# Kernel optimization log

Hardware: AMD Instinct MI355X
Metric: run time of the kernel (lower is better)

## Reference

```python
import jax, jax.numpy as jnp
import numpy as np
import math

TOPK = 13
ALPHA = 1.0
BETA = 6.0
EPS = 1e-9
NUM_CLASSES = 80
BG = NUM_CLASSES
IMG = 640.0


def _make_centers():
    # YOLO-style anchor-free grid at strides 8/16/32 for a 640x640 image -> L=8400
    pts = []
    for s, g in [(8, 80), (16, 40), (32, 20)]:
        xs = (np.arange(g) + 0.5) * s
        xv, yv = np.meshgrid(xs, xs)
        pts.append(np.stack([xv.ravel(), yv.ravel()], axis=-1))
    return jnp.asarray(np.concatenate(pts, 0), jnp.float32)


def _rand_boxes(kc, kw, shape, wmin, wmax):
    c = jax.random.uniform(kc, shape + (2,), minval=0.0, maxval=IMG)
    wh = jax.random.uniform(kw, shape + (2,), minval=wmin, maxval=wmax)
    return jnp.concatenate([c - wh / 2, c + wh / 2], axis=-1)


def setup_inputs() -> dict:
    key = jax.random.key(0)
    ks = jax.random.split(key, 8)
    B, L, C, n = 32, 8400, NUM_CLASSES, 64
    centers = _make_centers()                       # (L,2)
    pred_scores = jax.random.uniform(ks[0], (B, L, C))
    # predicted boxes centered near the grid cells
    noise = jax.random.normal(ks[1], (B, L, 2)) * 8.0
    pwh = jax.random.uniform(ks[2], (B, L, 2), minval=4.0, maxval=128.0)
    pc = centers[None] + noise
    pred_bboxes = jnp.concatenate([pc - pwh / 2, pc + pwh / 2], axis=-1)
    gt_bboxes = _rand_boxes(ks[3], ks[4], (B, n), 8.0, 256.0)
    gt_labels = jax.random.randint(ks[5], (B, n, 1), 0, NUM_CLASSES).astype(jnp.int32)
    counts = jax.random.randint(ks[6], (B,), 1, n + 1)
    pad_gt_mask = (jnp.arange(n)[None, :] < counts[:, None]).astype(jnp.float32)[..., None]
    return {"pred_scores": pred_scores, "pred_bboxes": pred_bboxes,
            "cell_centers_scaled": centers, "gt_labels": gt_labels,
            "gt_bboxes": gt_bboxes, "pad_gt_mask": pad_gt_mask}


def _ciou(b1, b2, eps=1e-7):
    # pairwise complete IoU: b1 (n,4) gt, b2 (L,4) pred -> (n,L). Matches torchvision.complete_box_iou.
    a1 = (b1[:, 2] - b1[:, 0]) * (b1[:, 3] - b1[:, 1])
    a2 = (b2[:, 2] - b2[:, 0]) * (b2[:, 3] - b2[:, 1])
    lt = jnp.maximum(b1[:, None, :2], b2[None, :, :2])
    rb = jnp.minimum(b1[:, None, 2:], b2[None, :, 2:])
    wh = jnp.clip(rb - lt, 0)
    inter = wh[..., 0] * wh[..., 1]
    union = a1[:, None] + a2[None, :] - inter
    iou = inter / union
    lti = jnp.minimum(b1[:, None, :2], b2[None, :, :2])
    rbi = jnp.maximum(b1[:, None, 2:], b2[None, :, 2:])
    whi = jnp.clip(rbi - lti, 0)
    diag2 = whi[..., 0] ** 2 + whi[..., 1] ** 2 + eps
    cx1 = (b1[:, 0] + b1[:, 2]) / 2; cy1 = (b1[:, 1] + b1[:, 3]) / 2
    cx2 = (b2[:, 0] + b2[:, 2]) / 2; cy2 = (b2[:, 1] + b2[:, 3]) / 2
    dist2 = (cx1[:, None] - cx2[None, :]) ** 2 + (cy1[:, None] - cy2[None, :]) ** 2
    diou = iou - dist2 / diag2
    w1 = b1[:, 2] - b1[:, 0]; h1 = b1[:, 3] - b1[:, 1]
    w2 = b2[:, 2] - b2[:, 0]; h2 = b2[:, 3] - b2[:, 1]
    v = (4.0 / math.pi ** 2) * (jnp.arctan(w1 / h1)[:, None] - jnp.arctan(w2 / h2)[None, :]) ** 2
    alpha = jax.lax.stop_gradient(v / (1 - iou + v + eps))
    return diou - alpha * v


def reference(pred_scores, pred_bboxes, cell_centers_scaled, gt_labels, gt_bboxes, pad_gt_mask):
    B, L, C = pred_scores.shape
    n = gt_bboxes.shape[1]
    # --- points-inside-gt check: (B,n,L) ---
    x = cell_centers_scaled[None, None, :, 0]
    y = cell_centers_scaled[None, None, :, 1]
    bb = gt_bboxes[:, :, None, :]
    ltrb_min = jnp.minimum(jnp.minimum(x - bb[..., 0], y - bb[..., 1]),
                           jnp.minimum(bb[..., 2] - x, bb[..., 3] - y))
    is_in_gts = (ltrb_min > EPS).astype(gt_bboxes.dtype)        # (B,n,L)
    # --- CIoU between each gt and each pred box ---
    ious = jax.vmap(_ciou)(gt_bboxes, pred_bboxes)              # (B,n,L)
    ious = jnp.clip(jnp.nan_to_num(ious, nan=0.0), 0)
    ious = ious * pad_gt_mask * is_in_gts
    # --- gather class score of each gt's label for every cell ---
    ps_t = jnp.swapaxes(pred_scores, 1, 2)                      # (B,C,L)
    gl = gt_labels.astype(jnp.int32)                            # (B,n,1)
    bbox_cls_scores = jnp.take_along_axis(ps_t, jnp.broadcast_to(gl, (B, n, L)), axis=1)
    alignment_metrics = bbox_cls_scores ** ALPHA * ious ** BETA # (B,n,L)
    # --- topk per gt, one-hot-sum style membership ---
    _, topk_idxs = jax.lax.top_k(alignment_metrics, TOPK)       # (B,n,TOPK)
    topk_mask = jnp.broadcast_to(pad_gt_mask > 0, topk_idxs.shape)
    topk_idxs = jnp.where(topk_mask, topk_idxs, 0)
    bi = jnp.arange(B)[:, None, None]
    ni = jnp.arange(n)[None, :, None]
    cnt = jnp.zeros((B, n, L), jnp.int32).at[bi, ni, topk_idxs].add(1)
    is_in_topk = jnp.where(cnt > 1, 0, cnt).astype(alignment_metrics.dtype)
    mask_positive = is_in_topk * is_in_gts * pad_gt_mask        # (B,n,L)
    mask_positive_sum = mask_positive.sum(axis=1)               # (B,L)
    # --- resolve cells assigned to multiple gts by max IoU (unconditional == torch's data-dependent branch) ---
    is_max_iou = (ious == ious.max(axis=1, keepdims=True)).astype(ious.dtype)
    mask_positive = jnp.where(mask_positive_sum[:, None, :] > 1, is_max_iou, mask_positive)
    mask_positive_sum = mask_positive.sum(axis=1)
    assigned_gt_index = jnp.argmax(mask_positive, axis=1)       # (B,L)
    assigned_labels = jnp.take_along_axis(gl[..., 0], assigned_gt_index, axis=1)
    assigned_labels = jnp.where(mask_positive_sum > 0, assigned_labels, BG)
    assigned_bboxes = jnp.take_along_axis(gt_bboxes, assigned_gt_index[..., None], axis=1)  # (B,L,4)
    assigned_scores = jax.nn.one_hot(assigned_labels, NUM_CLASSES + 1, dtype=pred_scores.dtype)[:, :, :NUM_CLASSES]
    # --- rescale scores by normalized alignment metric ---
    am = alignment_metrics * mask_positive
    max_metrics = am.max(axis=-1, keepdims=True)
    max_ious = (ious * mask_positive).max(axis=-1, keepdims=True)
    am = am / (max_metrics + EPS) * max_ious
    norm = am.max(axis=1)[..., None]                            # (B,L,1)
    assigned_scores = assigned_scores * norm
    foreground_mask = mask_positive_sum > 0
    return assigned_labels, assigned_bboxes, assigned_scores, foreground_mask
```

## Files before the change

### kernel.cpp

```cpp
#include <hip/hip_runtime.h>

#define BATCH 32
#define LANCH 8400
#define NCLS  80
#define NGT   64
#define TOPK  13
#define NCHUNK 33
#define CAP   1792
#define NPW   263

struct GtLds {
  float4 box[NGT];
  float  ga[NGT], gcx[NGT], gcy[NGT], atg[NGT], padf[NGT];
  int    lab[NGT];
};

__device__ __forceinline__ void load_gt(GtLds& s, int b,
    const float* gt_bboxes, const int* gt_labels, const float* pad_mask, int t)
{
  if (t < NGT) {
    float4 g = reinterpret_cast<const float4*>(gt_bboxes)[b * NGT + t];
    s.box[t] = g;
    float gw = g.z - g.x, gh = g.w - g.y;
    s.ga[t]  = gw * gh;
    s.gcx[t] = (g.x + g.z) * 0.5f;
    s.gcy[t] = (g.y + g.w) * 0.5f;
    s.atg[t] = atanf(gw / gh);
    s.padf[t] = pad_mask[b * NGT + t];
    s.lab[t]  = gt_labels[b * NGT + t];
  }
}

__device__ __forceinline__ float ciou_core(
    float4 pb, float pa, float pcx, float pcy, float atp,
    float4 gb, float ga, float gcx, float gcy, float atg)
{
  float iw = fmaxf(fminf(gb.z, pb.z) - fmaxf(gb.x, pb.x), 0.f);
  float ih = fmaxf(fminf(gb.w, pb.w) - fmaxf(gb.y, pb.y), 0.f);
  float inter = iw * ih;
  float uni   = ga + pa - inter;
  float iou   = inter / uni;
  float wi = fmaxf(fmaxf(gb.z, pb.z) - fminf(gb.x, pb.x), 0.f);
  float hi = fmaxf(fmaxf(gb.w, pb.w) - fminf(gb.y, pb.y), 0.f);
  float diag2 = wi * wi + hi * hi + 1e-7f;
  float dx = gcx - pcx, dy = gcy - pcy;
  float diou = iou - (dx * dx + dy * dy) / diag2;
  float dat = atg - atp;
  float v = 0.40528473456935109f * dat * dat;
  float alpha = v / (1.f - iou + v + 1e-7f);
  return fmaxf(diou - alpha * v, 0.f);
}

__device__ __forceinline__ float masked_ciou(
    float4 pb, float pa, float pcx, float pcy, float atp, float2 cc,
    float4 gb, float ga, float gcx, float gcy, float atg, float padf)
{
  float ltrb = fminf(fminf(cc.x - gb.x, cc.y - gb.y),
                     fminf(gb.z - cc.x, gb.w - cc.y));
  if (!(ltrb > 1e-9f) || padf == 0.f) return 0.f;
  return ciou_core(pb, pa, pcx, pcy, atp, gb, ga, gcx, gcy, atg);
}

__global__ __launch_bounds__(256) void k_rowtopk(
    const float* __restrict__ pred_scores,
    const float* __restrict__ pred_bboxes,
    const float* __restrict__ centers,
    const int*   __restrict__ gt_labels,
    const float* __restrict__ gt_bboxes,
    const float* __restrict__ pad_mask,
    unsigned long long* __restrict__ mask64)
{
  const int bg = blockIdx.x;
  if (pad_mask[bg] == 0.f) return;
  const int b = bg >> 6, g = bg & 63, t = threadIdx.x;

  __shared__ unsigned long long s_keys[CAP];
  __shared__ unsigned int       s_pos[NPW];
  __shared__ unsigned long long s_red[4];
  __shared__ unsigned long long s_kill;
  __shared__ int s_winl[TOPK];
  __shared__ int s_cnt;

  for (int i = t; i < NPW; i += 256) s_pos[i] = (i == NPW - 1) ? 0xFFFF0000u : 0u;
  if (t == 0) s_cnt = 0;

  const float4 gt = reinterpret_cast<const float4*>(gt_bboxes)[bg];
  const int   lab = gt_labels[bg];
  const float gw = gt.z - gt.x, gh = gt.w - gt.y;
  const float ga = gw * gh;
  const float gcx = (gt.x + gt.z) * 0.5f, gcy = (gt.y + gt.w) * 0.5f;
  const float atg = atanf(gw / gh);

  const int gdim[3] = {80, 40, 20};
  const int base[3] = {0, 6400, 8000};
  const float inv[3] = {0.125f, 0.0625f, 0.03125f};
  int i0[3], j0[3], w_[3], cum[4]; cum[0] = 0;
  for (int k = 0; k < 3; ++k) {
    int a0 = (int)floorf(gt.x * inv[k] - 0.5f) - 1; a0 = a0 < 0 ? 0 : a0;
    int a1 = (int)ceilf (gt.z * inv[k] - 0.5f) + 1; a1 = a1 > gdim[k] - 1 ? gdim[k] - 1 : a1;
    int b0 = (int)floorf(gt.y * inv[k] - 0.5f) - 1; b0 = b0 < 0 ? 0 : b0;
    int b1 = (int)ceilf (gt.w * inv[k] - 0.5f) + 1; b1 = b1 > gdim[k] - 1 ? gdim[k] - 1 : b1;
    i0[k] = a0; j0[k] = b0;
    int ww = a1 >= a0 ? a1 - a0 + 1 : 0;
    int hh = b1 >= b0 ? b1 - b0 + 1 : 0;
    w_[k] = ww;
    cum[k + 1] = cum[k] + ww * hh;
  }
  const int total = cum[3];
  const float2* cc2 = reinterpret_cast<const float2*>(centers);
  const float4* pb4 = reinterpret_cast<const float4*>(pred_bboxes) + (size_t)b * LANCH;
  const float*  sc  = pred_scores + (size_t)b * LANCH * NCLS + lab;
  __syncthreads();

  for (int c = t; c < total; c += 256) {
    int k = (c >= cum[1]) + (c >= cum[2]);
    int r = c - cum[k];
    int di = r % w_[k], dj = r / w_[k];
    int l = base[k] + (j0[k] + dj) * gdim[k] + (i0[k] + di);
    float2 cc = cc2[l];
    float ltrb = fminf(fminf(cc.x - gt.x, cc.y - gt.y),
                       fminf(gt.z - cc.x, gt.w - cc.y));
    if (!(ltrb > 1e-9f)) continue;
    float4 pb = pb4[l];
    float pw = pb.z - pb.x, ph = pb.w - pb.y, pa = pw * ph;
    float pcx = (pb.x + pb.z) * 0.5f, pcy = (pb.y + pb.w) * 0.5f;
    float atp = atanf(pw / ph);
    float io = ciou_core(pb, pa, pcx, pcy, atp, gt, ga, gcx, gcy, atg);
    float t2 = io * io;
    float met = sc[(size_t)l * NCLS] * (t2 * t2 * t2);
    if (met > 0.f) {
      int idx = atomicAdd(&s_cnt, 1);
      s_keys[idx] = ((unsigned long long)__float_as_uint(met) << 32)
                  | (unsigned int)(0x7FFFFFFF - l);
      atomicOr(&s_pos[l >> 5], 1u << (l & 31));
    }
  }
  __syncthreads();
  const int nnz  = s_cnt;
  const int npos = nnz < TOPK ? nnz : TOPK;
  const int w = t >> 6, lane = t & 63;

  unsigned long long mybest = 0;
  for (int i = t; i < nnz; i += 256) { unsigned long long v = s_keys[i]; if (v > mybest) mybest = v; }

  for (int it = 0; it < npos; ++it) {
    unsigned long long k = mybest;
    #pragma unroll
    for (int off = 32; off > 0; off >>= 1) {
      unsigned long long o = __shfl_down(k, off);
      if (o > k) k = o;
    }
    if (lane == 0) s_red[w] = k;
    __syncthreads();
    if (t == 0) {
      unsigned long long kk = s_red[0];
      if (s_red[1] > kk) kk = s_red[1];
      if (s_red[2] > kk) kk = s_red[2];
      if (s_red[3] > kk) kk = s_red[3];
      s_kill = kk;
      s_winl[it] = 0x7FFFFFFF - (int)(unsigned int)(kk & 0xFFFFFFFFu);
    }
    __syncthreads();
    unsigned long long kk = s_kill;
    bool own = false;
    for (int i = t; i < nnz; i += 256)
      if (s_keys[i] == kk) { s_keys[i] = 0; own = true; }
    if (own) {
      mybest = 0;
      for (int i = t; i < nnz; i += 256) { unsigned long long v = s_keys[i]; if (v > mybest) mybest = v; }
    }
    __syncthreads();
  }
  if (t == 0 && npos < TOPK) {
    int found = npos;
    for (int wd = 0; wd < NPW && found < TOPK; ++wd) {
      unsigned int z = ~s_pos[wd];
      while (z && found < TOPK) {
        int bit = __ffs(z) - 1; z &= z - 1;
        s_winl[found++] = wd * 32 + bit;
      }
    }
  }
  __syncthreads();
  if (t < TOPK) {
    int l = s_winl[t];
    float2 cc = cc2[l];
    float ltrb = fminf(fminf(cc.x - gt.x, cc.y - gt.y),
                       fminf(gt.z - cc.x, gt.w - cc.y));
    if (ltrb > 1e-9f)
      atomicOr(&mask64[(size_t)b * LANCH + l], 1ull << g);
  }
}

__global__ __launch_bounds__(256) void k_resolve(
    const float* __restrict__ pred_scores,
    const float* __restrict__ pred_bboxes,
    const float* __restrict__ centers,
    const int*   __restrict__ gt_labels,
    const float* __restrict__ gt_bboxes,
    const float* __restrict__ pad_mask,
    unsigned long long* __restrict__ mask64,
    float*       __restrict__ ws_mm,
    float*       __restrict__ ws_mi)
{
  __shared__ GtLds s;
  const int b = blockIdx.y, t = threadIdx.x;
  load_gt(s, b, gt_bboxes, gt_labels, pad_mask, t);
  __syncthreads();
  const int l = blockIdx.x * 256 + t;
  if (l >= LANCH) return;
  const int idx = b * LANCH + l;

  unsigned long long mb = mask64[idx];
  if (mb == 0ull) return;
  const int sum1 = __popcll(mb);

  const float4 pb = reinterpret_cast<const float4*>(pred_bboxes)[(size_t)b * LANCH + l];
  const float2 cc = reinterpret_cast<const float2*>(centers)[l];
  const float pw = pb.z - pb.x, ph = pb.w - pb.y;
  const float pa = pw * ph;
  const float pcx = (pb.x + pb.z) * 0.5f, pcy = (pb.y + pb.w) * 0.5f;
  const float atp = atanf(pw / ph);
  const float* srow = pred_scores + ((size_t)b * LANCH + l) * NCLS;

  unsigned long long fb = mb;
  if (sum1 > 1) {
    float mx = 0.f;
    unsigned long long eq = 0;
    for (int g = 0; g < NGT; ++g) {
      if (s.padf[g] == 0.f) break;
      float io = masked_ciou(pb, pa, pcx, pcy, atp, cc, s.box[g],
                             s.ga[g], s.gcx[g], s.gcy[g], s.atg[g], s.padf[g]);
      if (io > mx)       { mx = io; eq = 1ull << g; }
      else if (io == mx) { eq |= 1ull << g; }
    }
    fb = eq;
    mask64[idx] = eq;
  }

  unsigned long long bits = fb;
  while (bits) {
    int g = __ffsll((unsigned long long)bits) - 1;
    bits &= bits - 1;
    float io = masked_ciou(pb, pa, pcx, pcy, atp, cc, s.box[g],
                           s.ga[g], s.gcx[g], s.gcy[g], s.atg[g], s.padf[g]);
    float t2 = io * io;
    float met = srow[s.lab[g]] * (t2 * t2 * t2);
    atomicMax(reinterpret_cast<int*>(ws_mm + b * NGT + g), __float_as_int(met));
    atomicMax(reinterpret_cast<int*>(ws_mi + b * NGT + g), __float_as_int(io));
  }
}

__global__ __launch_bounds__(256) void k_write(
    const float* __restrict__ pred_scores,
    const float* __restrict__ pred_bboxes,
    const float* __restrict__ centers,
    const int*   __restrict__ gt_labels,
    const float* __restrict__ gt_bboxes,
    const float* __restrict__ pad_mask,
    const unsigned long long* __restrict__ mask64,
    const float* __restrict__ ws_mm,
    const float* __restrict__ ws_mi,
    float*       __restrict__ out_labels,
    float*       __restrict__ out_bboxes,
    float*       __restrict__ out_fg,
    float*       __restrict__ out_scores)
{
  __shared__ GtLds s;
  __shared__ float smm[NGT], smi[NGT];
  __shared__ float s_norm[256];
  __shared__ int   s_lab[256];
  const int b = blockIdx.y, t = threadIdx.x;
  load_gt(s, b, gt_bboxes, gt_labels, pad_mask, t);
  if (t < NGT) { smm[t] = ws_mm[b * NGT + t]; smi[t] = ws_mi[b * NGT + t]; }
  __syncthreads();
  const int l0 = blockIdx.x * 256;
  const int l  = l0 + t;
  const bool act = (l < LANCH);

  float norm = 0.f;
  int   lab  = NCLS;
  if (act) {
    const int idx = b * LANCH + l;
    unsigned long long bits = mask64[idx];
    if (bits != 0ull) {
      const float4 pb = reinterpret_cast<const float4*>(pred_bboxes)[(size_t)b * LANCH + l];
      const float2 cc = reinterpret_cast<const float2*>(centers)[l];
      const float pw = pb.z - pb.x, ph = pb.w - pb.y;
      const float pa = pw * ph;
      const float pcx = (pb.x + pb.z) * 0.5f, pcy = (pb.y + pb.w) * 0.5f;
      const float atp = atanf(pw / ph);
      const float* srow = pred_scores + ((size_t)b * LANCH + l) * NCLS;
      const int first = __ffsll((unsigned long long)bits) - 1;
      lab = s.lab[first];
      unsigned long long bb = bits;
      while (bb) {
        int g = __ffsll((unsigned long long)bb) - 1;
        bb &= bb - 1;
        float io = masked_ciou(pb, pa, pcx, pcy, atp, cc, s.box[g],
                               s.ga[g], s.gcx[g], s.gcy[g], s.atg[g], s.padf[g]);
        float t2 = io * io;
        float met = srow[s.lab[g]] * (t2 * t2 * t2);
        norm = fmaxf(norm, met / (smm[g] + 1e-9f) * smi[g]);
      }
      out_labels[idx] = (float)lab;
      reinterpret_cast<float4*>(out_bboxes)[idx] = s.box[first];
      out_fg[idx] = 1.f;
    } else {
      out_labels[idx] = (float)NCLS;
      reinterpret_cast<float4*>(out_bboxes)[idx] = s.box[0];
      out_fg[idx] = 0.f;
    }
  }
  s_norm[t] = norm;
  s_lab[t]  = lab;
  __syncthreads();

  const int QC = NCLS / 4;
  float4* tile = reinterpret_cast<float4*>(out_scores + ((size_t)b * LANCH + l0) * NCLS);
  const int amax = (LANCH - l0) < 256 ? (LANCH - l0) : 256;
  #pragma unroll
  for (int k = 0; k < QC; ++k) {
    int p = k * 256 + t;
    int a = p / QC, c4 = p - a * QC;
    if (a < amax) {
      float4 wv = make_float4(0.f, 0.f, 0.f, 0.f);
      int la = s_lab[a], base = c4 * 4;
      if (la >= base && la < base + 4) (&wv.x)[la - base] = s_norm[a];
      tile[p] = wv;
    }
  }
}

extern "C" void kernel_launch(void* const* d_in, const int* in_sizes, int n_in,
                              void* d_out, int out_size, void* d_ws, size_t ws_size,
                              hipStream_t stream) {
  const float* pred_scores = (const float*)d_in[0];
  const float* pred_bboxes = (const float*)d_in[1];
  const float* centers     = (const float*)d_in[2];
  const int*   gt_labels   = (const int*)  d_in[3];
  const float* gt_bboxes   = (const float*)d_in[4];
  const float* pad_mask    = (const float*)d_in[5];

  char* ws = (char*)d_ws;
  unsigned long long* mask64 = (unsigned long long*)ws;
  float* ws_mm = (float*)(ws + (size_t)BATCH * LANCH * 8);
  float* ws_mi = ws_mm + BATCH * NGT;
  const size_t zero_bytes = (size_t)BATCH * LANCH * 8 + 2 * BATCH * NGT * sizeof(float);

  float* out        = (float*)d_out;
  float* out_labels = out;
  float* out_bboxes = out + (size_t)BATCH * LANCH;
  float* out_scores = out + (size_t)BATCH * LANCH * 5;
  float* out_fg     = out + (size_t)BATCH * LANCH * 5 + (size_t)BATCH * LANCH * NCLS;

  hipMemsetAsync(ws, 0, zero_bytes, stream);

  k_rowtopk<<<BATCH * NGT, 256, 0, stream>>>(pred_scores, pred_bboxes, centers,
      gt_labels, gt_bboxes, pad_mask, mask64);

  dim3 grid(NCHUNK, BATCH);
  k_resolve<<<grid, 256, 0, stream>>>(pred_scores, pred_bboxes, centers,
      gt_labels, gt_bboxes, pad_mask, mask64, ws_mm, ws_mi);

  k_write<<<grid, 256, 0, stream>>>(pred_scores, pred_bboxes, centers,
      gt_labels, gt_bboxes, pad_mask, mask64, ws_mm, ws_mi,
      out_labels, out_bboxes, out_fg, out_scores);
}
```

Measured before the change: 227.0 us.

## Run per-GT top-k selection in a single wavefront without block barriers

The row top-k kernel now runs with one 64-lane wavefront per GT instead of 256 threads. Candidate keys are compacted into LDS with ballot and popcount prefix offsets instead of shared atomics. The iterative max extraction uses xor shuffles only, with no __syncthreads or cross-wave reduction. The position bitmap is dropped, and padding slots are filled by a linear scan against the winners list. This removes barrier and atomic overhead, but each block now has less parallelism for the CIoU candidate loop, and the LDS capacity grows to 2048 keys.

```diff
diff --git a/kernel.cpp b/kernel.cpp
--- a/kernel.cpp
+++ b/kernel.cpp
@@ -6,8 +6,7 @@
 #define NGT   64
 #define TOPK  13
 #define NCHUNK 33
-#define CAP   1792
-#define NPW   263
+#define CAP   2048
 
 struct GtLds {
   float4 box[NGT];
@@ -61,7 +60,11 @@
   return ciou_core(pb, pa, pcx, pcy, atp, gb, ga, gcx, gcy, atg);
 }
 
-__global__ __launch_bounds__(256) void k_rowtopk(
+__device__ __forceinline__ unsigned long long umax64(unsigned long long a,
+                                                     unsigned long long b)
+{ return a > b ? a : b; }
+
+__global__ __launch_bounds__(64) void k_rowtopk(
     const float* __restrict__ pred_scores,
     const float* __restrict__ pred_bboxes,
     const float* __restrict__ centers,
@@ -72,17 +75,10 @@
 {
   const int bg = blockIdx.x;
   if (pad_mask[bg] == 0.f) return;
-  const int b = bg >> 6, g = bg & 63, t = threadIdx.x;
+  const int b = bg >> 6, g = bg & 63, lane = threadIdx.x;
 
   __shared__ unsigned long long s_keys[CAP];
-  __shared__ unsigned int       s_pos[NPW];
-  __shared__ unsigned long long s_red[4];
-  __shared__ unsigned long long s_kill;
   __shared__ int s_winl[TOPK];
-  __shared__ int s_cnt;
-
-  for (int i = t; i < NPW; i += 256) s_pos[i] = (i == NPW - 1) ? 0xFFFF0000u : 0u;
-  if (t == 0) s_cnt = 0;
 
   const float4 gt = reinterpret_cast<const float4*>(gt_bboxes)[bg];
   const int   lab = gt_labels[bg];
@@ -110,80 +106,75 @@
   const float2* cc2 = reinterpret_cast<const float2*>(centers);
   const float4* pb4 = reinterpret_cast<const float4*>(pred_bboxes) + (size_t)b * LANCH;
   const float*  sc  = pred_scores + (size_t)b * LANCH * NCLS + lab;
-  __syncthreads();
-
-  for (int c = t; c < total; c += 256) {
-    int k = (c >= cum[1]) + (c >= cum[2]);
-    int r = c - cum[k];
-    int di = r % w_[k], dj = r / w_[k];
-    int l = base[k] + (j0[k] + dj) * gdim[k] + (i0[k] + di);
-    float2 cc = cc2[l];
-    float ltrb = fminf(fminf(cc.x - gt.x, cc.y - gt.y),
-                       fminf(gt.z - cc.x, gt.w - cc.y));
-    if (!(ltrb > 1e-9f)) continue;
-    float4 pb = pb4[l];
-    float pw = pb.z - pb.x, ph = pb.w - pb.y, pa = pw * ph;
-    float pcx = (pb.x + pb.z) * 0.5f, pcy = (pb.y + pb.w) * 0.5f;
-    float atp = atanf(pw / ph);
-    float io = ciou_core(pb, pa, pcx, pcy, atp, gt, ga, gcx, gcy, atg);
-    float t2 = io * io;
-    float met = sc[(size_t)l * NCLS] * (t2 * t2 * t2);
-    if (met > 0.f) {
-      int idx = atomicAdd(&s_cnt, 1);
-      s_keys[idx] = ((unsigned long long)__float_as_uint(met) << 32)
-                  | (unsigned int)(0x7FFFFFFF - l);
-      atomicOr(&s_pos[l >> 5], 1u << (l & 31));
-    }
-  }
-  __syncthreads();
-  const int nnz  = s_cnt;
+
+  int cnt = 0;
+  const unsigned long long lmask = (1ull << lane) - 1ull;
+  const int iters = (total + 63) >> 6;
+  for (int it = 0; it < iters; ++it) {
+    const int c = it * 64 + lane;
+    bool valid = false;
+    unsigned long long key = 0;
+    if (c < total) {
+      int k = (c >= cum[1]) + (c >= cum[2]);
+      int r = c - cum[k];
+      int di = r % w_[k], dj = r / w_[k];
+      int l = base[k] + (j0[k] + dj) * gdim[k] + (i0[k] + di);
+      float2 cc = cc2[l];
+      float ltrb = fminf(fminf(cc.x - gt.x, cc.y - gt.y),
+                         fminf(gt.z - cc.x, gt.w - cc.y));
+      if (ltrb > 1e-9f) {
+        float4 pb = pb4[l];
+        float pw = pb.z - pb.x, ph = pb.w - pb.y, pa = pw * ph;
+        float pcx = (pb.x + pb.z) * 0.5f, pcy = (pb.y + pb.w) * 0.5f;
+        float atp = atanf(pw / ph);
+        float io = ciou_core(pb, pa, pcx, pcy, atp, gt, ga, gcx, gcy, atg);
+        float t2 = io * io;
+        float met = sc[(size_t)l * NCLS] * (t2 * t2 * t2);
+        if (met > 0.f) {
+          valid = true;
+          key = ((unsigned long long)__float_as_uint(met) << 32)
+              | (unsigned int)(0x7FFFFFFF - l);
+        }
+      }
+    }
+    unsigned long long bal = __ballot(valid);
+    if (valid) s_keys[cnt + __popcll(bal & lmask)] = key;
+    cnt += __popcll(bal);
+  }
+  const int nnz  = cnt;
   const int npos = nnz < TOPK ? nnz : TOPK;
-  const int w = t >> 6, lane = t & 63;
 
   unsigned long long mybest = 0;
-  for (int i = t; i < nnz; i += 256) { unsigned long long v = s_keys[i]; if (v > mybest) mybest = v; }
+  for (int i = lane; i < nnz; i += 64) mybest = umax64(mybest, s_keys[i]);
 
   for (int it = 0; it < npos; ++it) {
     unsigned long long k = mybest;
     #pragma unroll
     for (int off = 32; off > 0; off >>= 1) {
-      unsigned long long o = __shfl_down(k, off);
+      unsigned long long o = __shfl_xor(k, off);
       if (o > k) k = o;
     }
-    if (lane == 0) s_red[w] = k;
-    __syncthreads();
-    if (t == 0) {
-      unsigned long long kk = s_red[0];
-      if (s_red[1] > kk) kk = s_red[1];
-      if (s_red[2] > kk) kk = s_red[2];
-      if (s_red[3] > kk) kk = s_red[3];
-      s_kill = kk;
-      s_winl[it] = 0x7FFFFFFF - (int)(unsigned int)(kk & 0xFFFFFFFFu);
-    }
-    __syncthreads();
-    unsigned long long kk = s_kill;
-    bool own = false;
-    for (int i = t; i < nnz; i += 256)
-      if (s_keys[i] == kk) { s_keys[i] = 0; own = true; }
-    if (own) {
+    if (lane == 0) s_winl[it] = 0x7FFFFFFF - (int)(unsigned int)(k & 0xFFFFFFFFu);
+    if (mybest == k) {
       mybest = 0;
-      for (int i = t; i < nnz; i += 256) { unsigned long long v = s_keys[i]; if (v > mybest) mybest = v; }
-    }
-    __syncthreads();
-  }
-  if (t == 0 && npos < TOPK) {
+      for (int i = lane; i < nnz; i += 64) {
+        unsigned long long v = s_keys[i];
+        if (v == k) { s_keys[i] = 0; v = 0; }
+        mybest = umax64(mybest, v);
+      }
+    }
+  }
+  if (lane == 0 && npos < TOPK) {
     int found = npos;
-    for (int wd = 0; wd < NPW && found < TOPK; ++wd) {
-      unsigned int z = ~s_pos[wd];
-      while (z && found < TOPK) {
-        int bit = __ffs(z) - 1; z &= z - 1;
-        s_winl[found++] = wd * 32 + bit;
-      }
+    for (int l = 0; found < TOPK && l < LANCH; ++l) {
+      bool taken = false;
+      for (int k = 0; k < npos; ++k) if (s_winl[k] == l) taken = true;
+      if (!taken) s_winl[found++] = l;
     }
   }
   __syncthreads();
-  if (t < TOPK) {
-    int l = s_winl[t];
+  if (lane < TOPK) {
+    int l = s_winl[lane];
     float2 cc = cc2[l];
     float ltrb = fminf(fminf(cc.x - gt.x, cc.y - gt.y),
                        fminf(gt.z - cc.x, gt.w - cc.y));
@@ -356,7 +347,7 @@
 
   hipMemsetAsync(ws, 0, zero_bytes, stream);
 
-  k_rowtopk<<<BATCH * NGT, 256, 0, stream>>>(pred_scores, pred_bboxes, centers,
+  k_rowtopk<<<BATCH * NGT, 64, 0, stream>>>(pred_scores, pred_bboxes, centers,
       gt_labels, gt_bboxes, pad_mask, mask64);
 
   dim3 grid(NCHUNK, BATCH);
```

Measured after the change: 230.3 us (median of 2 runs). No clear change (+1.4%).
